# Optimization experiments

Measured on AMD Instinct MI355X. Metric: run time of the kernel, lower is better.

## Reference

```python
import jax, jax.numpy as jnp
import numpy as np

ND, NP_, NC, H, L, B = 4000, 19000, 1000, 128, 2, 30000
E_DP, E_PP, E_CP = 200000, 300000, 150000


def setup_inputs() -> dict:
    key = jax.random.key(0)
    ks = iter(jax.random.split(key, 64))
    def nrm(shape, s=0.05):
        return jax.random.normal(next(ks), shape, dtype=jnp.float32) * s
    inp = {
        'drug_emb': nrm((ND, H)), 'protein_emb': nrm((NP_, H)), 'cell_emb': nrm((NC, H)),
    }
    for r in ['dp', 'rdp', 'pp', 'cp', 'rcp']:
        inp['W_' + r] = nrm((L, H, H))
        inp['a_src_' + r] = nrm((L, H))
        inp['a_dst_' + r] = nrm((L, H))
        inp['b_' + r] = jnp.zeros((L, H), jnp.float32)
    inp['W1'] = nrm((3 * H, 6 * H)); inp['b1'] = jnp.zeros((6 * H,), jnp.float32)
    inp['W2'] = nrm((6 * H, 2 * H)); inp['b2'] = jnp.zeros((2 * H,), jnp.float32)
    inp['W3'] = nrm((2 * H, 2)); inp['b3'] = jnp.zeros((2,), jnp.float32)
    def ri(n, hi):
        return jax.random.randint(next(ks), (n,), 0, hi, dtype=jnp.int32)
    inp['src_dp'] = ri(E_DP, ND); inp['dst_dp'] = ri(E_DP, NP_)
    inp['src_pp'] = ri(E_PP, NP_); inp['dst_pp'] = ri(E_PP, NP_)
    inp['src_cp'] = ri(E_CP, NC); inp['dst_cp'] = ri(E_CP, NP_)
    inp['drug1'] = ri(B, ND); inp['drug2'] = ri(B, ND); inp['cell'] = ri(B, NC)
    return inp


def _gat(x_src, x_dst, W, a_s, a_d, b, src, dst, n_dst):
    # Single-head PyG GATConv: shared linear, additive attention, segment softmax over dst.
    h_s = x_src @ W                      # [Ns, H]
    h_d = x_dst @ W                      # [Nd, H]
    e = jax.nn.leaky_relu((h_s @ a_s)[src] + (h_d @ a_d)[dst], 0.2)  # [E]
    m = jax.lax.stop_gradient(jax.ops.segment_max(e, dst, num_segments=n_dst))
    p = jnp.exp(e - m[dst])
    denom = jax.ops.segment_sum(p, dst, num_segments=n_dst)
    alpha = p / denom[dst]
    out = jax.ops.segment_sum(alpha[:, None] * h_s[src], dst, num_segments=n_dst)
    return out + b


def _l2norm(x):
    return x / jnp.maximum(jnp.linalg.norm(x, axis=1, keepdims=True), 1e-12)


def reference(drug_emb, protein_emb, cell_emb,
              W_dp, a_src_dp, a_dst_dp, b_dp,
              W_rdp, a_src_rdp, a_dst_rdp, b_rdp,
              W_pp, a_src_pp, a_dst_pp, b_pp,
              W_cp, a_src_cp, a_dst_cp, b_cp,
              W_rcp, a_src_rcp, a_dst_rcp, b_rcp,
              W1, b1, W2, b2, W3, b3,
              src_dp, dst_dp, src_pp, dst_pp, src_cp, dst_cp,
              drug1, drug2, cell):
    # p-p uses add_self_loops=True
    loops = jnp.arange(NP_, dtype=src_pp.dtype)
    spp = jnp.concatenate([src_pp, loops]); dpp = jnp.concatenate([dst_pp, loops])
    x_d, x_p, x_c = drug_emb, protein_emb, cell_emb
    for l in range(L):
        out_p = _gat(x_d, x_p, W_dp[l], a_src_dp[l], a_dst_dp[l], b_dp[l], src_dp, dst_dp, NP_)
        out_p = out_p + _gat(x_p, x_p, W_pp[l], a_src_pp[l], a_dst_pp[l], b_pp[l], spp, dpp, NP_)
        out_p = out_p + _gat(x_c, x_p, W_cp[l], a_src_cp[l], a_dst_cp[l], b_cp[l], src_cp, dst_cp, NP_)
        out_d = _gat(x_p, x_d, W_rdp[l], a_src_rdp[l], a_dst_rdp[l], b_rdp[l], dst_dp, src_dp, ND)
        out_c = _gat(x_p, x_c, W_rcp[l], a_src_rcp[l], a_dst_rcp[l], b_rcp[l], dst_cp, src_cp, NC)
        x_d, x_p, x_c = jax.nn.relu(out_d), jax.nn.relu(out_p), jax.nn.relu(out_c)
    hid = jnp.concatenate([_l2norm(x_d[drug1]), _l2norm(x_d[drug2]), _l2norm(x_c[cell])], axis=1)
    h = jax.nn.relu(hid @ W1 + b1)
    h = jax.nn.relu(h @ W2 + b2)
    return h @ W3 + b3
```

## Files before the change

kernel.cpp:

```cpp
#include <hip/hip_runtime.h>
#include <hip/hip_bf16.h>

#define H 128
#define ND 4000
#define NPN 19000
#define NCN 1000
#define NLAYERS 2
#define NB 30000
#define E_DP 200000
#define E_PP 300000
#define E_CP 150000

typedef __bf16 bf16_t;
typedef bf16_t bf16x8 __attribute__((ext_vector_type(8)));
typedef float f32x4 __attribute__((ext_vector_type(4)));
typedef unsigned short u16;

static __device__ __forceinline__ float wred_sum(float v) {
#pragma unroll
  for (int off = 32; off; off >>= 1) v += __shfl_xor(v, off);
  return v;
}
static __device__ __forceinline__ float bflo(unsigned u) { return __uint_as_float(u << 16); }
static __device__ __forceinline__ float bfhi(unsigned u) { return __uint_as_float(u & 0xffff0000u); }
static __device__ __forceinline__ unsigned packbf(float v0, float v1) {
  union { bf16_t b; unsigned short u; } a, b;
  a.b = (bf16_t)v0; b.b = (bf16_t)v1;
  return (unsigned)a.u | ((unsigned)b.u << 16);
}

#define GLDS16(gp, lp) \
  __builtin_amdgcn_global_load_lds((__attribute__((address_space(1))) void*)(gp), \
                                   (__attribute__((address_space(3))) void*)(lp), 16, 0, 0)

__device__ __forceinline__ void mfma_core(
    const bf16_t* __restrict__ A, const bf16_t* __restrict__ Bt,
    int M, int K, int ldb, int m0, int n0, f32x4 (&acc)[4][4])
{
  __shared__ char As[128 * 64];
  __shared__ char Bs[128 * 64];
  const int t = threadIdx.x;
  const int lane = t & 63;
#pragma unroll
  for (int mi = 0; mi < 4; ++mi)
#pragma unroll
    for (int ni = 0; ni < 4; ++ni) acc[mi][ni] = (f32x4){0.f, 0.f, 0.f, 0.f};

  const int wid = t >> 6;
  const int wr = wid >> 1, wc = wid & 1;
  const int sr = t >> 2;
  const int sc = t & 3;
  const int csrc = ((sc ^ ((sr >> 1) & 3)) << 4);
  int ra0 = m0 + sr;      if (ra0 >= M) ra0 = M - 1;
  int ra1 = m0 + 64 + sr; if (ra1 >= M) ra1 = M - 1;
  const char* gA0 = (const char*)A + (size_t)ra0 * K * 2 + csrc;
  const char* gA1 = (const char*)A + (size_t)ra1 * K * 2 + csrc;
  const char* gB0 = (const char*)Bt + (size_t)(n0 + sr) * ldb * 2 + csrc;
  const char* gB1 = (const char*)Bt + (size_t)(n0 + 64 + sr) * ldb * 2 + csrc;
  char* lA0 = As + t * 16;
  char* lA1 = As + 4096 + t * 16;
  char* lB0 = Bs + t * 16;
  char* lB1 = Bs + 4096 + t * 16;

  int aoff[4], boff[4];
#pragma unroll
  for (int mi = 0; mi < 4; ++mi) {
    int r = wr * 64 + mi * 16 + (lane & 15);
    aoff[mi] = r * 64 + ((((lane >> 4)) ^ ((r >> 1) & 3)) << 4);
  }
#pragma unroll
  for (int ni = 0; ni < 4; ++ni) {
    int r = wc * 64 + ni * 16 + (lane & 15);
    boff[ni] = r * 64 + ((((lane >> 4)) ^ ((r >> 1) & 3)) << 4);
  }

  for (int k0 = 0; k0 < K; k0 += 32) {
    const size_t kb = (size_t)k0 * 2;
    __syncthreads();
    GLDS16(gA0 + kb, lA0);
    GLDS16(gA1 + kb, lA1);
    GLDS16(gB0 + kb, lB0);
    GLDS16(gB1 + kb, lB1);
    __syncthreads();
    bf16x8 av[4], bv[4];
#pragma unroll
    for (int mi = 0; mi < 4; ++mi) av[mi] = *(const bf16x8*)(As + aoff[mi]);
#pragma unroll
    for (int ni = 0; ni < 4; ++ni) bv[ni] = *(const bf16x8*)(Bs + boff[ni]);
#pragma unroll
    for (int mi = 0; mi < 4; ++mi)
#pragma unroll
      for (int ni = 0; ni < 4; ++ni)
        acc[mi][ni] = __builtin_amdgcn_mfma_f32_16x16x32_bf16(av[mi], bv[ni], acc[mi][ni], 0, 0, 0);
  }
}

struct GJob { const bf16_t* A; const bf16_t* Bt; bf16_t* C; int M; int K;
              const float *b1, *b2, *b3; };
struct Gemm3 { GJob j[3]; };
__global__ __launch_bounds__(256) void k_gemm_g3(Gemm3 g) {
  const GJob& jb = g.j[blockIdx.y];
  int m0 = blockIdx.x * 128;
  if (m0 >= jb.M) return;
  f32x4 acc[4][4];
  mfma_core(jb.A, jb.Bt, jb.M, jb.K, jb.K, m0, 0, acc);
  const int t = threadIdx.x, lane = t & 63, wid = t >> 6;
  const int wr = wid >> 1, wc = wid & 1;
  const int col0 = lane & 15, rsub = (lane >> 4) * 4;
#pragma unroll
  for (int mi = 0; mi < 4; ++mi) {
#pragma unroll
    for (int ni = 0; ni < 4; ++ni) {
      int c = wc * 64 + ni * 16 + col0;
      float bb = jb.b1[c];
      if (jb.b2) bb += jb.b2[c];
      if (jb.b3) bb += jb.b3[c];
#pragma unroll
      for (int rg = 0; rg < 4; ++rg) {
        int r = m0 + wr * 64 + mi * 16 + rsub + rg;
        if (r < jb.M) jb.C[(size_t)r * H + c] = (bf16_t)fmaxf(acc[mi][ni][rg] + bb, 0.f);
      }
    }
  }
}

struct PJob { const bf16_t* A; bf16_t* C; int M; const float* rs; };
struct GemmPS { PJob j[3]; const bf16_t* Bt; const float* b1t; };
__global__ __launch_bounds__(256) void k_gemm_ps(GemmPS g) {
  const PJob& jb = g.j[blockIdx.y];
  int mt = blockIdx.x / 6, nt = blockIdx.x - mt * 6;
  int m0 = mt * 128;
  if (m0 >= jb.M) return;
  int n0 = nt * 128;
  f32x4 acc[4][4];
  mfma_core(jb.A, g.Bt + blockIdx.y * 128, jb.M, 128, 384, m0, n0, acc);
  const int t = threadIdx.x, lane = t & 63, wid = t >> 6;
  const int wr = wid >> 1, wc = wid & 1;
  const int col0 = lane & 15, rsub = (lane >> 4) * 4;
#pragma unroll
  for (int mi = 0; mi < 4; ++mi) {
#pragma unroll
    for (int rg = 0; rg < 4; ++rg) {
      int r = m0 + wr * 64 + mi * 16 + rsub + rg;
      if (r < jb.M) {
        float sc = jb.rs[r];
#pragma unroll
        for (int ni = 0; ni < 4; ++ni) {
          int c = n0 + wc * 64 + ni * 16 + col0;
          jb.C[(size_t)r * 768 + c] = (bf16_t)(acc[mi][ni][rg] * sc + g.b1t[c]);
        }
      }
    }
  }
}

__global__ __launch_bounds__(256) void k_w2head(
    const bf16_t* __restrict__ Pa, const bf16_t* __restrict__ Pb, const bf16_t* __restrict__ Pc,
    const int* __restrict__ d1, const int* __restrict__ d2, const int* __restrict__ ce,
    const bf16_t* __restrict__ W2t, const float* __restrict__ b2,
    const float* __restrict__ W3, const float* __restrict__ b3,
    float* __restrict__ out, int cn)
{
  __shared__ char As[128 * 64];
  __shared__ char Bs[256 * 64];
  const int t = threadIdx.x;
  const int lane = t & 63;
  const int m0 = blockIdx.x * 128;
  if (m0 >= cn) return;
  f32x4 acc[4][8];
#pragma unroll
  for (int mi = 0; mi < 4; ++mi)
#pragma unroll
    for (int ni = 0; ni < 8; ++ni) acc[mi][ni] = (f32x4){0.f, 0.f, 0.f, 0.f};

  const int arow = t >> 1;
  const int ah = t & 1;
  int gr = m0 + arow; if (gr >= cn) gr = cn - 1;
  const bf16_t* pa = Pa + (size_t)d1[gr] * 768 + ah * 16;
  const bf16_t* pb = Pb + (size_t)d2[gr] * 768 + ah * 16;
  const bf16_t* pc = Pc + (size_t)ce[gr] * 768 + ah * 16;
  const int swz = (arow >> 1) & 3;
  char* la0 = As + arow * 64 + (((ah * 2)     ^ swz) << 4);
  char* la1 = As + arow * 64 + (((ah * 2 + 1) ^ swz) << 4);

  const int sr = t >> 2;
  const int sc = t & 3;
  const int csrc = ((sc ^ ((sr >> 1) & 3)) << 4);
  const char* gB = (const char*)W2t + (size_t)sr * 768 * 2 + csrc;
  const size_t qstep = (size_t)64 * 768 * 2;

  const int wid = t >> 6;
  const int wr = wid >> 1, wc = wid & 1;
  int aoff[4], boff[8];
#pragma unroll
  for (int mi = 0; mi < 4; ++mi) {
    int r = wr * 64 + mi * 16 + (lane & 15);
    aoff[mi] = r * 64 + ((((lane >> 4)) ^ ((r >> 1) & 3)) << 4);
  }
#pragma unroll
  for (int ni = 0; ni < 8; ++ni) {
    int r = wc * 128 + ni * 16 + (lane & 15);
    boff[ni] = r * 64 + ((((lane >> 4)) ^ ((r >> 1) & 3)) << 4);
  }

#define ACC8(U, o) { s[o+0] += bflo(U.x); s[o+1] += bfhi(U.x); s[o+2] += bflo(U.y); s[o+3] += bfhi(U.y); \
                     s[o+4] += bflo(U.z); s[o+5] += bfhi(U.z); s[o+6] += bflo(U.w); s[o+7] += bfhi(U.w); }
  for (int k0 = 0; k0 < 768; k0 += 32) {
    uint4 Ua0 = *(const uint4*)(pa + k0);
    uint4 Ua1 = *(const uint4*)(pa + k0 + 8);
    uint4 Ub0 = *(const uint4*)(pb + k0);
    uint4 Ub1 = *(const uint4*)(pb + k0 + 8);
    uint4 Uc0 = *(const uint4*)(pc + k0);
    uint4 Uc1 = *(const uint4*)(pc + k0 + 8);
    float s[16] = {0.f, 0.f, 0.f, 0.f, 0.f, 0.f, 0.f, 0.f,
                   0.f, 0.f, 0.f, 0.f, 0.f, 0.f, 0.f, 0.f};
    ACC8(Ua0, 0) ACC8(Ua1, 8)
    ACC8(Ub0, 0) ACC8(Ub1, 8)
    ACC8(Uc0, 0) ACC8(Uc1, 8)
    uint4 P0, P1;
    P0.x = packbf(fmaxf(s[0], 0.f),  fmaxf(s[1], 0.f));
    P0.y = packbf(fmaxf(s[2], 0.f),  fmaxf(s[3], 0.f));
    P0.z = packbf(fmaxf(s[4], 0.f),  fmaxf(s[5], 0.f));
    P0.w = packbf(fmaxf(s[6], 0.f),  fmaxf(s[7], 0.f));
    P1.x = packbf(fmaxf(s[8], 0.f),  fmaxf(s[9], 0.f));
    P1.y = packbf(fmaxf(s[10], 0.f), fmaxf(s[11], 0.f));
    P1.z = packbf(fmaxf(s[12], 0.f), fmaxf(s[13], 0.f));
    P1.w = packbf(fmaxf(s[14], 0.f), fmaxf(s[15], 0.f));
    const size_t kb = (size_t)k0 * 2;
    __syncthreads();
    GLDS16(gB + kb,             Bs + t * 16);
    GLDS16(gB + qstep + kb,     Bs + 4096 + t * 16);
    GLDS16(gB + 2 * qstep + kb, Bs + 8192 + t * 16);
    GLDS16(gB + 3 * qstep + kb, Bs + 12288 + t * 16);
    *(uint4*)la0 = P0;
    *(uint4*)la1 = P1;
    __syncthreads();
    bf16x8 av[4], bv[8];
#pragma unroll
    for (int mi = 0; mi < 4; ++mi) av[mi] = *(const bf16x8*)(As + aoff[mi]);
#pragma unroll
    for (int ni = 0; ni < 8; ++ni) bv[ni] = *(const bf16x8*)(Bs + boff[ni]);
#pragma unroll
    for (int mi = 0; mi < 4; ++mi)
#pragma unroll
      for (int ni = 0; ni < 8; ++ni)
        acc[mi][ni] = __builtin_amdgcn_mfma_f32_16x16x32_bf16(av[mi], bv[ni], acc[mi][ni], 0, 0, 0);
  }
#undef ACC8

  const int col0 = lane & 15, rsub = (lane >> 4) * 4;
  float w0[8], w1[8], bb[8];
#pragma unroll
  for (int ni = 0; ni < 8; ++ni) {
    int c = wc * 128 + ni * 16 + col0;
    w0[ni] = W3[2 * c]; w1[ni] = W3[2 * c + 1]; bb[ni] = b2[c];
  }
#pragma unroll
  for (int mi = 0; mi < 4; ++mi) {
#pragma unroll
    for (int rg = 0; rg < 4; ++rg) {
      int r = m0 + wr * 64 + mi * 16 + rsub + rg;
      float p0 = 0.f, p1 = 0.f;
#pragma unroll
      for (int ni = 0; ni < 8; ++ni) {
        float v = fmaxf(acc[mi][ni][rg] + bb[ni], 0.f);
        p0 = fmaf(v, w0[ni], p0);
        p1 = fmaf(v, w1[ni], p1);
      }
#pragma unroll
      for (int off = 1; off < 16; off <<= 1) {
        p0 += __shfl_xor(p0, off);
        p1 += __shfl_xor(p1, off);
      }
      if (col0 == 0 && r < cn) {
        if (wc == 0) { p0 += b3[0]; p1 += b3[1]; }
        atomicAdd(&out[(size_t)r * 2], p0);
        atomicAdd(&out[(size_t)r * 2 + 1], p1);
      }
    }
  }
}

__global__ __launch_bounds__(256) void k_conv_emb(
    const float* __restrict__ xd, const float* __restrict__ xp, const float* __restrict__ xc,
    bf16_t* __restrict__ od, bf16_t* __restrict__ op, bf16_t* __restrict__ oc)
{
  int i = blockIdx.x * 256 + threadIdx.x;
  const int SD = ND * H, SP = NPN * H, SC = NCN * H;
  if (i < SD) od[i] = (bf16_t)xd[i];
  else if (i < SD + SP) op[i - SD] = (bf16_t)xp[i - SD];
  else if (i < SD + SP + SC) oc[i - SD - SP] = (bf16_t)xc[i - SD - SP];
}

__global__ __launch_bounds__(256) void k_scale3(const float* __restrict__ b1, float* __restrict__ o) {
  int i = blockIdx.x * 256 + threadIdx.x;
  if (i < 768) o[i] = b1[i] * (1.f / 3.f);
}

struct TC { const float* src[12]; bf16_t* dst[12]; int Ksub[12]; int N[12]; int Kfull[12]; int koff[12]; };
__global__ __launch_bounds__(256) void k_tconv2(TC a) {
  int m = blockIdx.z;
  int Ks = a.Ksub[m], N = a.N[m];
  int tx = blockIdx.x * 32;
  int ty = blockIdx.y * 32;
  if (tx >= N || ty >= Ks) return;
  __shared__ float tile[32][33];
  int c = threadIdx.x & 31, rr = threadIdx.x >> 5;
#pragma unroll
  for (int kk = rr; kk < 32; kk += 8)
    if (ty + kk < Ks && tx + c < N) tile[kk][c] = a.src[m][(size_t)(ty + kk) * N + tx + c];
  __syncthreads();
  bf16_t* dst = a.dst[m];
  int Kf = a.Kfull[m], ko = a.koff[m];
#pragma unroll
  for (int nn = rr; nn < 32; nn += 8)
    if (tx + nn < N && ty + c < Ks)
      dst[(size_t)(tx + nn) * Kf + ko + ty + c] = (bf16_t)tile[c][nn];
}

struct Wd20 { const float* W[20]; const float* a[20]; float* o[20]; };
__global__ __launch_bounds__(128) void k_wd20(Wd20 g) {
  int m = blockIdx.x;
  int k = threadIdx.x;
  const float* Wp = g.W[m];
  const float* av = g.a[m];
  float s = 0.f;
#pragma unroll 4
  for (int j = 0; j < H; ++j) s = fmaf(Wp[k * H + j], av[j], s);
  g.o[m][k] = s;
}

struct Sc { const bf16_t* xd; const bf16_t* xp; const bf16_t* xc; const float* wv;
            float* ss[5]; float* sd[5]; };
__global__ __launch_bounds__(256) void k_scores(Sc S) {
  int row = blockIdx.x * 4 + (threadIdx.x >> 6);
  if (row >= ND + NPN + NCN) return;
  int lane = threadIdx.x & 63;
  const bf16_t* x;
  int idx, cls;
  if (row < ND) { x = S.xd; idx = row; cls = 0; }
  else if (row < ND + NPN) { x = S.xp; idx = row - ND; cls = 1; }
  else { x = S.xc; idx = row - ND - NPN; cls = 2; }
  unsigned u = *(const unsigned*)(x + (size_t)idx * H + lane * 2);
  float x0 = bflo(u), x1 = bfhi(u);
  const float* wv = S.wv;
#define DOT(vi, outp) { const float* v = wv + (vi) * H; \
    float s = x0 * v[2 * lane] + x1 * v[2 * lane + 1]; s = wred_sum(s); \
    if (!lane) (outp)[idx] = s; }
  if (cls == 0) {
    DOT(0, S.ss[0]); DOT(8, S.sd[3]);
  } else if (cls == 1) {
    DOT(1, S.ss[1]); DOT(3, S.ss[3]); DOT(4, S.ss[4]);
    DOT(5, S.sd[0]); DOT(6, S.sd[1]); DOT(7, S.sd[2]);
  } else {
    DOT(2, S.ss[2]); DOT(9, S.sd[4]);
  }
#undef DOT
}

struct CsrArgs {
  const int* src[5]; const int* dst[5];
  int E[5]; int n[5];
  int* cnt[5]; int* cur[5]; int* starts[5]; u16* csr[5];
};
__global__ __launch_bounds__(256) void k_count5(CsrArgs a) {
  int rel = blockIdx.y;
  int E = a.E[rel];
  const int* dst = a.dst[rel];
  int* cnt = a.cnt[rel];
  int e0 = blockIdx.x * 1024 + threadIdx.x;
#pragma unroll
  for (int u = 0; u < 4; ++u) {
    int e = e0 + u * 256;
    if (e < E) atomicAdd(&cnt[dst[e]], 1);
  }
}
__global__ __launch_bounds__(1024) void k_scan5(CsrArgs a) {
  int rel = blockIdx.x;
  int n = a.n[rel];
  const int* cnt = a.cnt[rel];
  int* st = a.starts[rel];
  int* cu = a.cur[rel];
  int t = threadIdx.x;
  int stripe = (n + 1023) / 1024;
  int lo = t * stripe;
  int hi = lo + stripe; if (hi > n) hi = n;
  int s = 0;
  for (int i = lo; i < hi; ++i) s += cnt[i];
  int lane = t & 63, wv = t >> 6;
  int x = s;
#pragma unroll
  for (int off = 1; off < 64; off <<= 1) {
    int y = __shfl_up(x, off);
    if (lane >= off) x += y;
  }
  __shared__ int ws[16];
  if (lane == 63) ws[wv] = x;
  __syncthreads();
  if (t == 0) {
    int run = 0;
#pragma unroll
    for (int i = 0; i < 16; ++i) { int v = ws[i]; ws[i] = run; run += v; }
  }
  __syncthreads();
  int run = ws[wv] + x - s;
  for (int i = lo; i < hi; ++i) { st[i] = run; cu[i] = run; run += cnt[i]; }
  if (t == 1023) st[n] = ws[15] + x;
}
__global__ __launch_bounds__(256) void k_fill5(CsrArgs a) {
  int rel = blockIdx.y;
  int E = a.E[rel];
  const int* dst = a.dst[rel];
  const int* src = a.src[rel];
  int* cur = a.cur[rel];
  u16* csr = a.csr[rel];
  int e0 = blockIdx.x * 1024 + threadIdx.x;
#pragma unroll
  for (int u = 0; u < 4; ++u) {
    int e = e0 + u * 256;
    if (e < E) {
      int pos = atomicAdd(&cur[dst[e]], 1);
      csr[pos] = (u16)src[e];
    }
  }
}

struct Agg5 {
  const u16* csr[5]; const int* starts[5];
  const float* ss[5]; const float* sd[5];
  const bf16_t* xs[5];
  bf16_t* y[5]; int ystride[5]; int ycoff[5]; int ndst[5]; int self[5];
};
__global__ __launch_bounds__(256) void k_agg5(Agg5 a) {
  int rel = blockIdx.y;
  int d = blockIdx.x * 4 + (threadIdx.x >> 6);
  if (d >= a.ndst[rel]) return;
  int lane = threadIdx.x & 63;
  int g = lane >> 4, j16 = lane & 15;
  bf16_t* yrow = a.y[rel] + (size_t)d * a.ystride[rel] + a.ycoff[rel];
  int s0 = a.starts[rel][d];
  int deg = a.starts[rel][d + 1] - s0;
  int selfa = a.self[rel];
  if (!deg && !selfa) {
    if (g == 0) *(uint4*)(yrow + j16 * 8) = make_uint4(0u, 0u, 0u, 0u);
    return;
  }
  const u16* cs = a.csr[rel] + s0;
  const float* ssp = a.ss[rel];
  const bf16_t* xsp = a.xs[rel];
  float sdv = a.sd[rel][d];
  float acc[8] = {0.f, 0.f, 0.f, 0.f, 0.f, 0.f, 0.f, 0.f};
  float ps = 0.f;
  for (int b = 0; b < deg; b += 16) {
#pragma unroll
    for (int u = 0; u < 4; ++u) {
      int i = b + u * 4 + g;
      float p = 0.f;
      uint4 U = make_uint4(0u, 0u, 0u, 0u);
      if (i < deg) {
        int s = cs[i];
        float e = ssp[s] + sdv; e = e > 0.f ? e : 0.2f * e;
        p = __expf(e);
        U = *(const uint4*)(xsp + (size_t)s * H + j16 * 8);
      }
      ps += p;
      acc[0] = fmaf(p, bflo(U.x), acc[0]); acc[1] = fmaf(p, bfhi(U.x), acc[1]);
      acc[2] = fmaf(p, bflo(U.y), acc[2]); acc[3] = fmaf(p, bfhi(U.y), acc[3]);
      acc[4] = fmaf(p, bflo(U.z), acc[4]); acc[5] = fmaf(p, bfhi(U.z), acc[5]);
      acc[6] = fmaf(p, bflo(U.w), acc[6]); acc[7] = fmaf(p, bfhi(U.w), acc[7]);
    }
  }
  if (selfa && g == 0) {
    float e = ssp[d] + sdv; e = e > 0.f ? e : 0.2f * e;
    float p = __expf(e);
    uint4 U = *(const uint4*)(xsp + (size_t)d * H + j16 * 8);
    ps += p;
    acc[0] = fmaf(p, bflo(U.x), acc[0]); acc[1] = fmaf(p, bfhi(U.x), acc[1]);
    acc[2] = fmaf(p, bflo(U.y), acc[2]); acc[3] = fmaf(p, bfhi(U.y), acc[3]);
    acc[4] = fmaf(p, bflo(U.z), acc[4]); acc[5] = fmaf(p, bfhi(U.z), acc[5]);
    acc[6] = fmaf(p, bflo(U.w), acc[6]); acc[7] = fmaf(p, bfhi(U.w), acc[7]);
  }
#pragma unroll
  for (int e = 0; e < 8; ++e) {
    acc[e] += __shfl_xor(acc[e], 16);
    acc[e] += __shfl_xor(acc[e], 32);
  }
  ps += __shfl_xor(ps, 16);
  ps += __shfl_xor(ps, 32);
  if (g == 0) {
    float inv = 1.f / ps;
    uint4 O;
    O.x = packbf(acc[0] * inv, acc[1] * inv);
    O.y = packbf(acc[2] * inv, acc[3] * inv);
    O.z = packbf(acc[4] * inv, acc[5] * inv);
    O.w = packbf(acc[6] * inv, acc[7] * inv);
    *(uint4*)(yrow + j16 * 8) = O;
  }
}

__global__ __launch_bounds__(256) void k_invnorm(
    const bf16_t* __restrict__ xd, const bf16_t* __restrict__ xc,
    float* __restrict__ invd, float* __restrict__ invc)
{
  int row = blockIdx.x * 4 + (threadIdx.x >> 6);
  if (row >= ND + NCN) return;
  int lane = threadIdx.x & 63;
  const bf16_t* x = (row < ND) ? xd + (size_t)row * H : xc + (size_t)(row - ND) * H;
  unsigned u = ((const unsigned*)x)[lane];
  float av = bflo(u), bv = bfhi(u);
  float s = wred_sum(av * av + bv * bv);
  if (!lane) {
    float nv = fmaxf(sqrtf(s), 1e-12f);
    if (row < ND) invd[row] = 1.f / nv; else invc[row - ND] = 1.f / nv;
  }
}

extern "C" void kernel_launch(void* const* d_in, const int* in_sizes, int n_in,
                              void* d_out, int out_size, void* d_ws, size_t ws_size,
                              hipStream_t stream)
{
  (void)in_sizes; (void)n_in;
  const float* drug_emb    = (const float*)d_in[0];
  const float* protein_emb = (const float*)d_in[1];
  const float* cell_emb    = (const float*)d_in[2];
  const int base_idx[5] = {3, 11, 15, 7, 19};
  const float *W_[5], *as_[5], *ad_[5], *b_[5];
  for (int r = 0; r < 5; ++r) {
    W_[r]  = (const float*)d_in[base_idx[r]];
    as_[r] = (const float*)d_in[base_idx[r] + 1];
    ad_[r] = (const float*)d_in[base_idx[r] + 2];
    b_[r]  = (const float*)d_in[base_idx[r] + 3];
  }
  const float* W1 = (const float*)d_in[23]; const float* b1 = (const float*)d_in[24];
  const float* W2 = (const float*)d_in[25]; const float* b2 = (const float*)d_in[26];
  const float* W3 = (const float*)d_in[27]; const float* b3 = (const float*)d_in[28];
  const int* src_dp = (const int*)d_in[29]; const int* dst_dp = (const int*)d_in[30];
  const int* src_pp = (const int*)d_in[31]; const int* dst_pp = (const int*)d_in[32];
  const int* src_cp = (const int*)d_in[33]; const int* dst_cp = (const int*)d_in[34];
  const int* drug1  = (const int*)d_in[35]; const int* drug2  = (const int*)d_in[36];
  const int* cellb  = (const int*)d_in[37];
  float* out = (float*)d_out;

  char* wsb = (char*)d_ws;
  size_t off = 0;
  auto alloc = [&](size_t bytes) -> void* {
    void* p = wsb + off;
    off += (bytes + 255) & ~(size_t)255;
    return p;
  };
  bf16_t* xdb[2] = {(bf16_t*)alloc((size_t)ND * H * 2),  (bf16_t*)alloc((size_t)ND * H * 2)};
  bf16_t* xpb[2] = {(bf16_t*)alloc((size_t)NPN * H * 2), (bf16_t*)alloc((size_t)NPN * H * 2)};
  bf16_t* xcb[2] = {(bf16_t*)alloc((size_t)NCN * H * 2), (bf16_t*)alloc((size_t)NCN * H * 2)};
  const int Msrc[5] = {ND, NPN, NCN, NPN, NPN};
  const int Mdst[5] = {NPN, NPN, NPN, ND, NCN};
  const int Erel[5] = {E_DP, E_PP, E_CP, E_DP, E_CP};
  bf16_t* yp = (bf16_t*)alloc((size_t)NPN * 384 * 2);
  bf16_t* yd = (bf16_t*)alloc((size_t)ND * H * 2);
  bf16_t* yc = (bf16_t*)alloc((size_t)NCN * H * 2);
  bf16_t* Wtp = (bf16_t*)alloc((size_t)NLAYERS * 128 * 384 * 2);
  bf16_t* Wtd = (bf16_t*)alloc((size_t)NLAYERS * 128 * 128 * 2);
  bf16_t* Wtc = (bf16_t*)alloc((size_t)NLAYERS * 128 * 128 * 2);
  bf16_t* W1t = (bf16_t*)alloc((size_t)768 * 384 * 2);
  bf16_t* W2t = (bf16_t*)alloc((size_t)256 * 768 * 2);
  float* wvb = (float*)alloc(20 * H * 4);
  float* b1t = (float*)alloc(768 * 4);
  float* ssb[5]; for (int r = 0; r < 5; ++r) ssb[r] = (float*)alloc((size_t)Msrc[r] * 4);
  float* sdb[5]; for (int r = 0; r < 5; ++r) sdb[r] = (float*)alloc((size_t)Mdst[r] * 4);
  int* cnt_all = (int*)alloc(62000 * 4);
  int* cur_all = (int*)alloc(62000 * 4);
  int* st_all  = (int*)alloc((62000 + 5) * 4);
  int *cntb[5], *curb[5], *stb[5];
  { int o = 0, o2 = 0;
    for (int r = 0; r < 5; ++r) {
      cntb[r] = cnt_all + o; curb[r] = cur_all + o; stb[r] = st_all + o2;
      o += Mdst[r]; o2 += Mdst[r] + 1;
    } }
  u16* csrb[5]; for (int r = 0; r < 5; ++r) csrb[r] = (u16*)alloc((size_t)Erel[r] * 2);
  float* invd = (float*)alloc(ND * 4);
  float* invc = (float*)alloc(NCN * 4);
  bf16_t* P1a = (bf16_t*)alloc((size_t)ND * 768 * 2);
  bf16_t* P1b = (bf16_t*)alloc((size_t)ND * 768 * 2);
  bf16_t* P1c = (bf16_t*)alloc((size_t)NCN * 768 * 2);
  (void)ws_size;

  hipMemsetAsync(out, 0, (size_t)out_size * 4, stream);

  k_conv_emb<<<(ND * H + NPN * H + NCN * H + 255) / 256, 256, 0, stream>>>(
      drug_emb, protein_emb, cell_emb, xdb[0], xpb[0], xcb[0]);
  k_scale3<<<3, 256, 0, stream>>>(b1, b1t);
  TC tc;
  for (int l = 0; l < 2; ++l) {
    for (int r = 0; r < 3; ++r) {
      int m = l * 3 + r;
      tc.src[m] = W_[r] + (size_t)l * H * H;
      tc.dst[m] = Wtp + (size_t)l * 128 * 384;
      tc.Ksub[m] = 128; tc.N[m] = 128; tc.Kfull[m] = 384; tc.koff[m] = r * 128;
    }
    tc.src[6 + l] = W_[3] + (size_t)l * H * H; tc.dst[6 + l] = Wtd + (size_t)l * 128 * 128;
    tc.Ksub[6 + l] = 128; tc.N[6 + l] = 128; tc.Kfull[6 + l] = 128; tc.koff[6 + l] = 0;
    tc.src[8 + l] = W_[4] + (size_t)l * H * H; tc.dst[8 + l] = Wtc + (size_t)l * 128 * 128;
    tc.Ksub[8 + l] = 128; tc.N[8 + l] = 128; tc.Kfull[8 + l] = 128; tc.koff[8 + l] = 0;
  }
  tc.src[10] = W1; tc.dst[10] = W1t; tc.Ksub[10] = 384; tc.N[10] = 768; tc.Kfull[10] = 384; tc.koff[10] = 0;
  tc.src[11] = W2; tc.dst[11] = W2t; tc.Ksub[11] = 768; tc.N[11] = 256; tc.Kfull[11] = 768; tc.koff[11] = 0;
  k_tconv2<<<dim3(24, 24, 12), 256, 0, stream>>>(tc);

  Wd20 wg;
  for (int l = 0; l < 2; ++l)
    for (int r = 0; r < 5; ++r) {
      int m = l * 10 + r;
      wg.W[m] = W_[r] + (size_t)l * H * H; wg.a[m] = as_[r] + l * H; wg.o[m] = wvb + m * H;
      int m2 = l * 10 + 5 + r;
      wg.W[m2] = W_[r] + (size_t)l * H * H; wg.a[m2] = ad_[r] + l * H; wg.o[m2] = wvb + m2 * H;
    }
  k_wd20<<<20, 128, 0, stream>>>(wg);

  hipMemsetAsync(cnt_all, 0, 62000 * 4, stream);
  CsrArgs ca;
  const int* srcA[5] = {src_dp, src_pp, src_cp, dst_dp, dst_cp};
  const int* dstA[5] = {dst_dp, dst_pp, dst_cp, src_dp, src_cp};
  for (int r = 0; r < 5; ++r) {
    ca.src[r] = srcA[r]; ca.dst[r] = dstA[r]; ca.E[r] = Erel[r]; ca.n[r] = Mdst[r];
    ca.cnt[r] = cntb[r]; ca.cur[r] = curb[r]; ca.starts[r] = stb[r]; ca.csr[r] = csrb[r];
  }
  dim3 egrid((E_PP + 1023) / 1024, 5);
  k_count5<<<egrid, 256, 0, stream>>>(ca);
  k_scan5<<<5, 1024, 0, stream>>>(ca);
  k_fill5<<<egrid, 256, 0, stream>>>(ca);

  int cur = 0;
  for (int l = 0; l < NLAYERS; ++l) {
    int nxt = 1 - cur;
    const bf16_t* xsrc[5] = {xdb[cur], xpb[cur], xcb[cur], xpb[cur], xpb[cur]};
    Sc sc;
    sc.xd = xdb[cur]; sc.xp = xpb[cur]; sc.xc = xcb[cur]; sc.wv = wvb + l * 10 * H;
    for (int r = 0; r < 5; ++r) { sc.ss[r] = ssb[r]; sc.sd[r] = sdb[r]; }
    k_scores<<<(ND + NPN + NCN + 3) / 4, 256, 0, stream>>>(sc);
    Agg5 aa;
    bf16_t* yptr[5] = {yp, yp, yp, yd, yc};
    const int ystr[5] = {384, 384, 384, 128, 128};
    const int ycof[5] = {0, 128, 256, 0, 0};
    const int selfs[5] = {0, 1, 0, 0, 0};
    for (int r = 0; r < 5; ++r) {
      aa.csr[r] = csrb[r]; aa.starts[r] = stb[r]; aa.ss[r] = ssb[r]; aa.sd[r] = sdb[r];
      aa.xs[r] = xsrc[r]; aa.y[r] = yptr[r]; aa.ystride[r] = ystr[r]; aa.ycoff[r] = ycof[r];
      aa.ndst[r] = Mdst[r]; aa.self[r] = selfs[r];
    }
    k_agg5<<<dim3((NPN + 3) / 4, 5), 256, 0, stream>>>(aa);
    Gemm3 g3;
    g3.j[0] = {yp, Wtp + (size_t)l * 128 * 384, xpb[nxt], NPN, 384,
               b_[0] + l * H, b_[1] + l * H, b_[2] + l * H};
    g3.j[1] = {yd, Wtd + (size_t)l * 128 * 128, xdb[nxt], ND, 128,
               b_[3] + l * H, nullptr, nullptr};
    g3.j[2] = {yc, Wtc + (size_t)l * 128 * 128, xcb[nxt], NCN, 128,
               b_[4] + l * H, nullptr, nullptr};
    k_gemm_g3<<<dim3((NPN + 127) / 128, 3), 256, 0, stream>>>(g3);
    cur = nxt;
  }

  k_invnorm<<<(ND + NCN + 3) / 4, 256, 0, stream>>>(xdb[cur], xcb[cur], invd, invc);
  GemmPS ps;
  ps.Bt = W1t; ps.b1t = b1t;
  ps.j[0] = {xdb[cur], P1a, ND, invd};
  ps.j[1] = {xdb[cur], P1b, ND, invd};
  ps.j[2] = {xcb[cur], P1c, NCN, invc};
  k_gemm_ps<<<dim3(32 * 6, 3), 256, 0, stream>>>(ps);
  k_w2head<<<(NB + 127) / 128, 256, 0, stream>>>(
      P1a, P1b, P1c, drug1, drug2, cellb, W2t, b2, W3, b3, out, NB);
}
```

Before: 400.6 us.

## Build CSR with destination-windowed blocks using LDS atomics

Replaces the global-atomic count and fill kernels with windowed kernels. Each of 32 blocks per relation owns a slice of destination nodes and scans the whole edge list, using shared-memory atomic counters and cursors. This drops the memset and the global cur array and avoids global atomic contention. In exchange every block rereads the full edge arrays, so edge reads grow 32-fold, and only 160 blocks run, which may leave the GPU underused.

Result: slower. 1.093 ms (+172.8%).

```diff
diff --git a/kernel.cpp b/kernel.cpp
--- a/kernel.cpp
+++ b/kernel.cpp
@@ -10,6 +10,8 @@
 #define E_DP 200000
 #define E_PP 300000
 #define E_CP 150000
+#define NW 32
+#define WSMAX 608
 
 typedef __bf16 bf16_t;
 typedef bf16_t bf16x8 __attribute__((ext_vector_type(8)));
@@ -358,29 +360,41 @@
 #undef DOT
 }
 
-struct CsrArgs {
+struct CsrW {
   const int* src[5]; const int* dst[5];
-  int E[5]; int n[5];
-  int* cnt[5]; int* cur[5]; int* starts[5]; u16* csr[5];
+  int E[5]; int n[5]; int ws[5];
+  int* cnt[5]; int* starts[5]; u16* csr[5];
 };
-__global__ __launch_bounds__(256) void k_count5(CsrArgs a) {
+__global__ __launch_bounds__(256) void k_countw(CsrW a) {
   int rel = blockIdx.y;
+  int ws = a.ws[rel], n = a.n[rel];
+  int w0 = blockIdx.x * ws;
+  if (w0 >= n) return;
+  int wn = n - w0; if (wn > ws) wn = ws;
+  __shared__ int lcnt[WSMAX];
+  for (int i = threadIdx.x; i < wn; i += 256) lcnt[i] = 0;
+  __syncthreads();
+  const int* dst = a.dst[rel];
   int E = a.E[rel];
-  const int* dst = a.dst[rel];
+  for (int base = 0; base < E; base += 1024) {
+#pragma unroll
+    for (int u = 0; u < 4; ++u) {
+      int e = base + u * 256 + threadIdx.x;
+      if (e < E) {
+        int d = dst[e] - w0;
+        if ((unsigned)d < (unsigned)wn) atomicAdd(&lcnt[d], 1);
+      }
+    }
+  }
+  __syncthreads();
   int* cnt = a.cnt[rel];
-  int e0 = blockIdx.x * 1024 + threadIdx.x;
-#pragma unroll
-  for (int u = 0; u < 4; ++u) {
-    int e = e0 + u * 256;
-    if (e < E) atomicAdd(&cnt[dst[e]], 1);
-  }
-}
-__global__ __launch_bounds__(1024) void k_scan5(CsrArgs a) {
+  for (int i = threadIdx.x; i < wn; i += 256) cnt[w0 + i] = lcnt[i];
+}
+__global__ __launch_bounds__(1024) void k_scan5(CsrW a) {
   int rel = blockIdx.x;
   int n = a.n[rel];
   const int* cnt = a.cnt[rel];
   int* st = a.starts[rel];
-  int* cu = a.cur[rel];
   int t = threadIdx.x;
   int stripe = (n + 1023) / 1024;
   int lo = t * stripe;
@@ -404,23 +418,34 @@
   }
   __syncthreads();
   int run = ws[wv] + x - s;
-  for (int i = lo; i < hi; ++i) { st[i] = run; cu[i] = run; run += cnt[i]; }
+  for (int i = lo; i < hi; ++i) { st[i] = run; run += cnt[i]; }
   if (t == 1023) st[n] = ws[15] + x;
 }
-__global__ __launch_bounds__(256) void k_fill5(CsrArgs a) {
+__global__ __launch_bounds__(256) void k_fillw(CsrW a) {
   int rel = blockIdx.y;
-  int E = a.E[rel];
+  int ws = a.ws[rel], n = a.n[rel];
+  int w0 = blockIdx.x * ws;
+  if (w0 >= n) return;
+  int wn = n - w0; if (wn > ws) wn = ws;
+  __shared__ int lcur[WSMAX];
+  const int* st = a.starts[rel];
+  for (int i = threadIdx.x; i < wn; i += 256) lcur[i] = st[w0 + i];
+  __syncthreads();
   const int* dst = a.dst[rel];
   const int* src = a.src[rel];
-  int* cur = a.cur[rel];
   u16* csr = a.csr[rel];
-  int e0 = blockIdx.x * 1024 + threadIdx.x;
-#pragma unroll
-  for (int u = 0; u < 4; ++u) {
-    int e = e0 + u * 256;
-    if (e < E) {
-      int pos = atomicAdd(&cur[dst[e]], 1);
-      csr[pos] = (u16)src[e];
+  int E = a.E[rel];
+  for (int base = 0; base < E; base += 1024) {
+#pragma unroll
+    for (int u = 0; u < 4; ++u) {
+      int e = base + u * 256 + threadIdx.x;
+      if (e < E) {
+        int d = dst[e] - w0;
+        if ((unsigned)d < (unsigned)wn) {
+          int pos = atomicAdd(&lcur[d], 1);
+          csr[pos] = (u16)src[e];
+        }
+      }
     }
   }
 }
@@ -567,12 +592,11 @@
   float* ssb[5]; for (int r = 0; r < 5; ++r) ssb[r] = (float*)alloc((size_t)Msrc[r] * 4);
   float* sdb[5]; for (int r = 0; r < 5; ++r) sdb[r] = (float*)alloc((size_t)Mdst[r] * 4);
   int* cnt_all = (int*)alloc(62000 * 4);
-  int* cur_all = (int*)alloc(62000 * 4);
   int* st_all  = (int*)alloc((62000 + 5) * 4);
-  int *cntb[5], *curb[5], *stb[5];
+  int *cntb[5], *stb[5];
   { int o = 0, o2 = 0;
     for (int r = 0; r < 5; ++r) {
-      cntb[r] = cnt_all + o; curb[r] = cur_all + o; stb[r] = st_all + o2;
+      cntb[r] = cnt_all + o; stb[r] = st_all + o2;
       o += Mdst[r]; o2 += Mdst[r] + 1;
     } }
   u16* csrb[5]; for (int r = 0; r < 5; ++r) csrb[r] = (u16*)alloc((size_t)Erel[r] * 2);
@@ -615,18 +639,17 @@
     }
   k_wd20<<<20, 128, 0, stream>>>(wg);
 
-  hipMemsetAsync(cnt_all, 0, 62000 * 4, stream);
-  CsrArgs ca;
+  CsrW cw;
   const int* srcA[5] = {src_dp, src_pp, src_cp, dst_dp, dst_cp};
   const int* dstA[5] = {dst_dp, dst_pp, dst_cp, src_dp, src_cp};
   for (int r = 0; r < 5; ++r) {
-    ca.src[r] = srcA[r]; ca.dst[r] = dstA[r]; ca.E[r] = Erel[r]; ca.n[r] = Mdst[r];
-    ca.cnt[r] = cntb[r]; ca.cur[r] = curb[r]; ca.starts[r] = stb[r]; ca.csr[r] = csrb[r];
-  }
-  dim3 egrid((E_PP + 1023) / 1024, 5);
-  k_count5<<<egrid, 256, 0, stream>>>(ca);
-  k_scan5<<<5, 1024, 0, stream>>>(ca);
-  k_fill5<<<egrid, 256, 0, stream>>>(ca);
+    cw.src[r] = srcA[r]; cw.dst[r] = dstA[r]; cw.E[r] = Erel[r]; cw.n[r] = Mdst[r];
+    cw.ws[r] = (Mdst[r] + NW - 1) / NW;
+    cw.cnt[r] = cntb[r]; cw.starts[r] = stb[r]; cw.csr[r] = csrb[r];
+  }
+  k_countw<<<dim3(NW, 5), 256, 0, stream>>>(cw);
+  k_scan5<<<5, 1024, 0, stream>>>(cw);
+  k_fillw<<<dim3(NW, 5), 256, 0, stream>>>(cw);
 
   int cur = 0;
   for (int l = 0; l < NLAYERS; ++l) {
```
